# Kernel tuning notes

Measured on AMD Instinct MI355X. Metric: run time of the kernel, lower is better.

## Reference

```python
import jax, jax.numpy as jnp
import numpy as np

D_MODEL = 1024
D_STATE = 64
D_CONV = 4
EXPAND = 2
INNER = EXPAND * D_STATE          # 128
PROJ = D_STATE + 2 * INNER        # 320
B, L = 8, 4096
EPS = 1e-4


def setup_inputs() -> dict:
    key = jax.random.key(0)
    ks = jax.random.split(key, 6)
    x = jax.random.normal(ks[0], (B, L, D_MODEL), dtype=jnp.float32)
    # depthwise conv weight, torch layout (out=D, in/group=1, K)
    conv_w = jax.random.normal(ks[1], (D_MODEL, 1, D_CONV), dtype=jnp.float32) / np.sqrt(D_CONV)
    conv_b = jnp.zeros((D_MODEL,), dtype=jnp.float32)
    in_proj_w = jax.random.normal(ks[2], (PROJ, D_MODEL), dtype=jnp.float32) / np.sqrt(D_MODEL)
    in_proj_b = jnp.zeros((PROJ,), dtype=jnp.float32)
    A_log = jax.random.normal(ks[3], (D_STATE,), dtype=jnp.float32) * 0.1
    out_proj_w = jax.random.normal(ks[4], (D_MODEL, D_STATE), dtype=jnp.float32) / np.sqrt(D_STATE)
    out_proj_b = jnp.zeros((D_MODEL,), dtype=jnp.float32)
    return {"x": x, "conv_w": conv_w, "conv_b": conv_b,
            "in_proj_w": in_proj_w, "in_proj_b": in_proj_b,
            "A_log": A_log, "out_proj_w": out_proj_w, "out_proj_b": out_proj_b}


def _ssm_forward(x, conv_w, conv_b, in_proj_w, in_proj_b, A_log, out_proj_w, out_proj_b):
    bsz, L_in, _ = x.shape
    # depthwise conv1d, padding (D_CONV-1)//2 on both sides (torch semantics)
    pad = (D_CONV - 1) // 2
    xc = jnp.transpose(x, (0, 2, 1))  # (B, D, L)
    xc = jax.lax.conv_general_dilated(
        xc, conv_w, window_strides=(1,), padding=[(pad, pad)],
        dimension_numbers=("NCH", "OIH", "NCH"), feature_group_count=D_MODEL)
    xc = xc + conv_b[None, :, None]
    Lc = xc.shape[2]
    if Lc < L_in:  # K even -> conv output is L-1; pad zeros on the right
        xc = jnp.pad(xc, ((0, 0), (0, 0), (0, L_in - Lc)))
    elif Lc > L_in:
        xc = xc[:, :, :L_in]
    xc = jnp.transpose(xc, (0, 2, 1))  # (B, L, D)

    proj = xc @ in_proj_w.T + in_proj_b  # (B, L, PROJ)
    delta = proj[..., :D_STATE]                                  # (B, L, N)
    B_in = proj[..., D_STATE:D_STATE + INNER]
    C = proj[..., D_STATE + INNER:]
    n_groups = INNER // D_STATE
    B_in = B_in.reshape(bsz, L_in, D_STATE, n_groups).mean(axis=-1)  # (B, L, N)
    C = C.reshape(bsz, L_in, D_STATE, n_groups).mean(axis=-1)        # (B, L, N)

    # ZOH discretization
    A = -jnp.exp(A_log)[None, None, :]          # (1, 1, N)
    delta = jax.nn.softplus(delta)
    dA = delta * A
    A_bar = jnp.exp(dA)                         # (B, L, N)
    A_safe = jnp.where(jnp.abs(A) < EPS, EPS * jnp.sign(A) + EPS, A)
    scale = (A_bar - 1.0) / A_safe
    taylor = 1.0 + dA / 2.0 + dA * dA / 6.0
    scale = jnp.where(jnp.abs(A) < EPS, taylor, scale)
    B_bar = scale * B_in                        # (B, L, N)

    # linear recurrence h_t = A_bar_t * h_{t-1} + B_bar_t via associative scan
    def comb(e1, e2):
        a1, b1 = e1
        a2, b2 = e2
        return a1 * a2, a2 * b1 + b2
    _, h = jax.lax.associative_scan(comb, (A_bar, B_bar), axis=1)  # (B, L, N)

    y_state = C * h
    return y_state @ out_proj_w.T + out_proj_b  # (B, L, D)


def reference(x, conv_w, conv_b, in_proj_w, in_proj_b, A_log, out_proj_w, out_proj_b):
    return _ssm_forward(x, conv_w, conv_b, in_proj_w, in_proj_b, A_log, out_proj_w, out_proj_b)
```

## Files before the change

### kernel.cpp

```cpp
#include <hip/hip_runtime.h>
#include <cstdint>
#include <cstddef>

typedef __bf16 bf16;
typedef __attribute__((ext_vector_type(4))) __bf16 bf16x4;
typedef __attribute__((ext_vector_type(8))) __bf16 bf16x8;
typedef __attribute__((ext_vector_type(4))) float f32x4;

#define EPS_C 1e-4f
#define SWZ(r) (((r) ^ ((r) >> 2)) & 3)

#define BAR_LDS() do { asm volatile("s_waitcnt lgkmcnt(0)" ::: "memory"); \
                       __builtin_amdgcn_s_barrier(); } while (0)

__global__ __launch_bounds__(256) void k0_prep(const float* __restrict__ Wi,
    const float* __restrict__ Wo, bf16* __restrict__ Whg, bf16* __restrict__ Wlg,
    bf16* __restrict__ Wob, float* __restrict__ zpg)
{
    int idx = blockIdx.x * 256 + threadIdx.x;
    if (idx < 196608) {
        int nn = idx >> 10, k = idx & 1023;
        int wn = nn / 48, s = nn - wn * 48;
        if (s < 16) {
            int d = wn * 16 + s;
            float w = Wi[d * 1024 + k];
            bf16 h = (bf16)w;
            Whg[(k >> 5) * 6144 + nn * 32 + (k & 31)] = h;
            Wlg[(k >> 5) * 2048 + d * 32 + (k & 31)] = (bf16)(w - (float)h);
        } else if (s < 32) {
            int i = wn * 16 + (s - 16);
            float w = 0.5f * (Wi[(64 + 2 * i) * 1024 + k] + Wi[(65 + 2 * i) * 1024 + k]);
            Whg[(k >> 5) * 6144 + nn * 32 + (k & 31)] = (bf16)w;
        } else {
            int i = wn * 16 + (s - 32);
            float w = 0.5f * (Wi[(192 + 2 * i) * 1024 + k] + Wi[(193 + 2 * i) * 1024 + k]);
            Whg[(k >> 5) * 6144 + nn * 32 + (k & 31)] = (bf16)w;
        }
    } else if (idx < 262144) {
        int j = idx - 196608;
        Wob[j] = (bf16)Wo[j];
    } else {
        int j = idx - 262144;
        if (j < 1024) zpg[j] = 0.f;
    }
}

__global__ __launch_bounds__(256, 4) void k1_convproj(
    const float* __restrict__ x, const float* __restrict__ conv_w,
    const float* __restrict__ conv_b, const float* __restrict__ in_proj_b,
    const float* __restrict__ A_log,
    const bf16* __restrict__ Whg, const bf16* __restrict__ Wlg,
    const float* __restrict__ zpg,
    float* __restrict__ Yp, float* __restrict__ Zp,
    float* __restrict__ Psum, float* __restrict__ Ssum)
{
    __shared__ char smem[28672];

    const int tid  = threadIdx.x;
    const int lane = tid & 63;
    const int wn   = tid >> 6;
    const int fr   = lane & 15, fs = lane >> 4;
    const int b    = blockIdx.x >> 7;
    const int tc   = blockIdx.x & 127;
    const int t0   = tc * 32;
    const int rot  = (blockIdx.x * 5) & 31;

    const int ct = tid >> 3, cs = tid & 7;
    const int gt = t0 + ct;
    const bool zrow = (gt == 4095);
    const int xwo = ct * 64 + ((((cs >> 1) ^ SWZ(ct)) & 3) << 4) + (cs & 1) * 8;

    int aoff[2];
#pragma unroll
    for (int mi = 0; mi < 2; ++mi) {
        int r = mi * 16 + fr;
        aoff[mi] = r * 64 + ((fs ^ SWZ(r)) << 4);
    }

    const float* rp[4];
#pragma unroll
    for (int dt = 0; dt < 4; ++dt) {
        int g = gt - 1 + dt;
        rp[dt] = (g >= 0 && g < 4096) ? (x + ((size_t)b * 4096 + g) * 1024 + cs * 4)
                                      : (zpg + cs * 4);
    }

    const size_t wfo  = (size_t)(wn * 48 + fr) * 32 + fs * 8;
    const size_t wfol = (size_t)(wn * 16 + fr) * 32 + fs * 8;

    {
        float* cwT = (float*)(smem + 8192);
        float* cbl = (float*)(smem + 24576);
        for (int p = tid; p < 1024; p += 256) {
            f32x4 w4 = *(const f32x4*)&conv_w[p * 4];
            cwT[p]        = w4.x;
            cwT[1024 + p] = w4.y;
            cwT[2048 + p] = w4.z;
            cwT[3072 + p] = w4.w;
        }
        ((f32x4*)cbl)[tid] = ((const f32x4*)conv_b)[tid];
    }

    f32x4  xr[4];
    bf16x8 wfh[3], wfl;
    f32x4  acc[2][3] = {};

    auto L = [&](int c) { return (c + rot) & 31; };

    auto fetch_x = [&](int lc) {
#pragma unroll
        for (int dt = 0; dt < 4; ++dt)
            xr[dt] = *(const f32x4*)(rp[dt] + lc * 32);
    };
    auto fetch_w = [&](int lc) {
        const bf16* ph = Whg + (size_t)lc * 6144 + wfo;
#pragma unroll
        for (int ni = 0; ni < 3; ++ni)
            wfh[ni] = *(const bf16x8*)(ph + ni * 512);
        wfl = *(const bf16x8*)(Wlg + (size_t)lc * 2048 + wfol);
    };
    auto conv = [&](int lc, int p) {
        char* xh = smem + p * 2048;
        char* xl = smem + 4096 + p * 2048;
        const float* cwT = (const float*)(smem + 8192);
        const float* cbl = (const float*)(smem + 24576);
        const int ch0 = lc * 32 + cs * 4;
        f32x4 w0 = *(const f32x4*)&cwT[ch0];
        f32x4 w1 = *(const f32x4*)&cwT[1024 + ch0];
        f32x4 w2 = *(const f32x4*)&cwT[2048 + ch0];
        f32x4 w3 = *(const f32x4*)&cwT[3072 + ch0];
        f32x4 bb = *(const f32x4*)&cbl[ch0];
        bf16x4 hi, lo;
#pragma unroll
        for (int j = 0; j < 4; ++j) {
            float v = bb[j];
            v = fmaf(w0[j], xr[0][j], v);
            v = fmaf(w1[j], xr[1][j], v);
            v = fmaf(w2[j], xr[2][j], v);
            v = fmaf(w3[j], xr[3][j], v);
            v = zrow ? 0.f : v;
            bf16 h = (bf16)v;
            hi[j] = h;
            lo[j] = (bf16)(v - (float)h);
        }
        *(bf16x4*)(xh + xwo) = hi;
        *(bf16x4*)(xl + xwo) = lo;
    };

    fetch_x(L(0));
    fetch_w(L(0));
    __syncthreads();
    conv(L(0), 0);
    fetch_x(L(1));
    __syncthreads();

    auto body = [&](int c, int par) {
        const char* xh = smem + par * 2048;
        const char* xl = smem + 4096 + par * 2048;
        bf16x8 ah0 = *(const bf16x8*)(xh + aoff[0]);
        bf16x8 ah1 = *(const bf16x8*)(xh + aoff[1]);
        bf16x8 al0 = *(const bf16x8*)(xl + aoff[0]);
        bf16x8 al1 = *(const bf16x8*)(xl + aoff[1]);
        __builtin_amdgcn_s_setprio(1);
#pragma unroll
        for (int ni = 0; ni < 3; ++ni) {
            bf16x8 bh = wfh[ni];
            acc[0][ni] = __builtin_amdgcn_mfma_f32_16x16x32_bf16(ah0, bh, acc[0][ni], 0, 0, 0);
            acc[1][ni] = __builtin_amdgcn_mfma_f32_16x16x32_bf16(ah1, bh, acc[1][ni], 0, 0, 0);
            acc[0][ni] = __builtin_amdgcn_mfma_f32_16x16x32_bf16(al0, bh, acc[0][ni], 0, 0, 0);
            acc[1][ni] = __builtin_amdgcn_mfma_f32_16x16x32_bf16(al1, bh, acc[1][ni], 0, 0, 0);
        }
        acc[0][0] = __builtin_amdgcn_mfma_f32_16x16x32_bf16(ah0, wfl, acc[0][0], 0, 0, 0);
        acc[1][0] = __builtin_amdgcn_mfma_f32_16x16x32_bf16(ah1, wfl, acc[1][0], 0, 0, 0);
        __builtin_amdgcn_s_setprio(0);
        if (c + 1 < 32) {
            fetch_w(L(c + 1));
            conv(L(c + 1), par ^ 1);
            if (c + 2 < 32) fetch_x(L(c + 2));
        }
        BAR_LDS();
    };

#pragma unroll 1
    for (int cc = 0; cc < 32; cc += 2) {
        body(cc,     0);
        body(cc + 1, 1);
    }

    float* res = (float*)smem;
#pragma unroll
    for (int mi = 0; mi < 2; ++mi)
#pragma unroll
        for (int ni = 0; ni < 3; ++ni) {
            int col = wn * 48 + ni * 16 + fr;
#pragma unroll
            for (int r = 0; r < 4; ++r)
                res[(mi * 16 + fs * 4 + r) * 196 + col] = acc[mi][ni][r];
        }
    __syncthreads();

    float* part = (float*)(smem + 25088);
    const int i  = lane;
    const int tg = tid >> 6;
    const float A  = -expf(A_log[i]);
    const float bd = in_proj_b[i];
    const float bB = 0.5f * (in_proj_b[64 + 2 * i] + in_proj_b[65 + 2 * i]);
    const float bC = 0.5f * (in_proj_b[192 + 2 * i] + in_proj_b[193 + 2 * i]);
    const bool tiny = fabsf(A) < EPS_C;
    const int dcol = (i >> 4) * 48 + (i & 15);
    float av[8], bv[8], cv[8];
#pragma unroll
    for (int r = 0; r < 8; ++r) {
        int t = tg * 8 + r;
        float d  = res[t * 196 + dcol] + bd;
        float Bm = res[t * 196 + dcol + 16] + bB;
        float Cm = res[t * 196 + dcol + 32] + bC;
        float delta = (d > 20.f) ? d : log1pf(expf(d));
        float dA = delta * A;
        float abar = expf(dA);
        float sc = tiny ? (1.f + dA * 0.5f + dA * dA * (1.f / 6.f)) : ((abar - 1.f) / A);
        av[r] = abar; bv[r] = sc * Bm; cv[r] = Cm;
    }
    float P = 1.f, S = 0.f;
#pragma unroll
    for (int r = 0; r < 8; ++r) { S = fmaf(av[r], S, bv[r]); P *= av[r]; }
    part[tg * 64 + i] = P;
    part[256 + tg * 64 + i] = S;
    __syncthreads();
    float h = 0.f, pp = 1.f;
#pragma unroll
    for (int g = 0; g < 3; ++g)
        if (g < tg) {
            float Pg = part[g * 64 + i], Sg = part[256 + g * 64 + i];
            h = fmaf(Pg, h, Sg);
            pp *= Pg;
        }
    size_t ob = ((size_t)b * 4096 + t0 + tg * 8) * 64 + i;
#pragma unroll
    for (int r = 0; r < 8; ++r) {
        h  = fmaf(av[r], h, bv[r]);
        pp *= av[r];
        Yp[ob + (size_t)r * 64] = cv[r] * h;
        Zp[ob + (size_t)r * 64] = cv[r] * pp;
    }
    if (tg == 3) {
        size_t o = ((size_t)b * 128 + tc) * 64 + i;
        Psum[o] = pp;
        Ssum[o] = h;
    }
}

__global__ __launch_bounds__(64) void k2_scan2(const float* __restrict__ Psum,
    const float* __restrict__ Ssum, float* __restrict__ Carry)
{
    int b = blockIdx.x, i = threadIdx.x;
    float h = 0.f;
#pragma unroll 1
    for (int g = 0; g < 8; ++g) {
        size_t base = ((size_t)b * 128 + g * 16) * 64 + i;
        float Pv[16], Sv[16];
#pragma unroll
        for (int j = 0; j < 16; ++j) {
            Pv[j] = Psum[base + (size_t)j * 64];
            Sv[j] = Ssum[base + (size_t)j * 64];
        }
#pragma unroll
        for (int j = 0; j < 16; ++j) {
            Carry[base + (size_t)j * 64] = h;
            h = fmaf(Pv[j], h, Sv[j]);
        }
    }
}

__global__ __launch_bounds__(512) void k3_scan_out(
    const float* __restrict__ Yp, const float* __restrict__ Zp,
    const float* __restrict__ Carry, const bf16* __restrict__ Wob,
    const float* __restrict__ bo, float* __restrict__ out)
{
    __shared__ char sm3[4096];

    const int tid  = threadIdx.x;
    const int lane = tid & 63;
    const int wv   = tid >> 6;
    const int b    = blockIdx.x >> 7;
    const int ch   = blockIdx.x & 127;
    const int t0   = ch * 32;

    const int i = lane, tg = wv;
    float cr = Carry[((size_t)b * 128 + ch) * 64 + i];
    size_t base = ((size_t)b * 4096 + t0 + tg * 4) * 64 + i;
#pragma unroll
    for (int r = 0; r < 4; ++r) {
        float y = Yp[base + (size_t)r * 64] + Zp[base + (size_t)r * 64] * cr;
        int t = tg * 4 + r;
        int off = t * 128 + ((((i >> 3) ^ (t & 7)) & 7) << 4) + (i & 7) * 2;
        *(bf16*)(sm3 + off) = (bf16)y;
    }
    __syncthreads();

    const int fr = lane & 15, fs = lane >> 4;
    bf16x8 afr[2][2];
#pragma unroll
    for (int mi = 0; mi < 2; ++mi)
#pragma unroll
        for (int ks = 0; ks < 2; ++ks) {
            int row = mi * 16 + fr;
            int slot = ks * 4 + fs;
            int off = row * 128 + (((slot ^ (row & 7)) & 7) << 4);
            afr[mi][ks] = *(const bf16x8*)(sm3 + off);
        }
    const int n0 = wv * 128;
#pragma unroll
    for (int ni = 0; ni < 8; ++ni) {
        int col = n0 + ni * 16 + fr;
        bf16x8 b0 = *(const bf16x8*)(Wob + (size_t)col * 64 + fs * 8);
        bf16x8 b1 = *(const bf16x8*)(Wob + (size_t)col * 64 + 32 + fs * 8);
        float bias = bo[col];
#pragma unroll
        for (int mi = 0; mi < 2; ++mi) {
            f32x4 a = {};
            a = __builtin_amdgcn_mfma_f32_16x16x32_bf16(afr[mi][0], b0, a, 0, 0, 0);
            a = __builtin_amdgcn_mfma_f32_16x16x32_bf16(afr[mi][1], b1, a, 0, 0, 0);
#pragma unroll
            for (int r = 0; r < 4; ++r) {
                int t = mi * 16 + fs * 4 + r;
                out[((size_t)b * 4096 + t0 + t) * 1024 + col] = a[r] + bias;
            }
        }
    }
}

extern "C" void kernel_launch(void* const* d_in, const int* in_sizes, int n_in,
                              void* d_out, int out_size, void* d_ws, size_t ws_size,
                              hipStream_t stream) {
    const float* x          = (const float*)d_in[0];
    const float* conv_w     = (const float*)d_in[1];
    const float* conv_b     = (const float*)d_in[2];
    const float* in_proj_w  = (const float*)d_in[3];
    const float* in_proj_b  = (const float*)d_in[4];
    const float* A_log      = (const float*)d_in[5];
    const float* out_proj_w = (const float*)d_in[6];
    const float* out_proj_b = (const float*)d_in[7];
    float* out = (float*)d_out;

    char* w = (char*)d_ws;
    bf16*  Whg  = (bf16*)w;
    bf16*  Wlg  = (bf16*)(w + 393216);
    bf16*  Wob  = (bf16*)(w + 524288);
    float* Yp   = (float*)(w + 655360);
    float* Zp   = (float*)(w + 9043968);
    float* Psum = (float*)(w + 17432576);
    float* Ssum = (float*)(w + 17694720);
    float* Carry= (float*)(w + 17956864);
    float* zpg  = (float*)(w + 18219008);

    hipLaunchKernelGGL(k0_prep,     dim3(1032), dim3(256), 0, stream,
                       in_proj_w, out_proj_w, Whg, Wlg, Wob, zpg);
    hipLaunchKernelGGL(k1_convproj, dim3(1024), dim3(256), 0, stream,
                       x, conv_w, conv_b, in_proj_b, A_log, Whg, Wlg, zpg,
                       Yp, Zp, Psum, Ssum);
    hipLaunchKernelGGL(k2_scan2,    dim3(8),    dim3(64),  0, stream, Psum, Ssum, Carry);
    hipLaunchKernelGGL(k3_scan_out, dim3(1024), dim3(512), 0, stream,
                       Yp, Zp, Carry, Wob, out_proj_b, out);
}
```

Before: 113.2 us.

## Double time-tile per block to 64 rows, halving grid and chunk count

Each convproj and scan_out block now covers 64 timesteps instead of 32, so every loaded weight fragment feeds four MFMA row tiles instead of two, and each thread converts 8 channels per step. The grid shrinks to 512 blocks and the carry scan handles 64 chunks per batch in one unrolled pass. This raises weight reuse and cuts redundant conv halo loads. In exchange it uses more LDS and registers per block and launches fewer blocks, which lowers occupancy and may underfill the 256 CUs.

```diff
diff --git a/kernel.cpp b/kernel.cpp
--- a/kernel.cpp
+++ b/kernel.cpp
@@ -3,7 +3,6 @@
 #include <cstddef>
 
 typedef __bf16 bf16;
-typedef __attribute__((ext_vector_type(4))) __bf16 bf16x4;
 typedef __attribute__((ext_vector_type(8))) __bf16 bf16x8;
 typedef __attribute__((ext_vector_type(4))) float f32x4;
 
@@ -45,7 +44,7 @@
     }
 }
 
-__global__ __launch_bounds__(256, 4) void k1_convproj(
+__global__ __launch_bounds__(256) void k1_convproj(
     const float* __restrict__ x, const float* __restrict__ conv_w,
     const float* __restrict__ conv_b, const float* __restrict__ in_proj_b,
     const float* __restrict__ A_log,
@@ -54,25 +53,25 @@
     float* __restrict__ Yp, float* __restrict__ Zp,
     float* __restrict__ Psum, float* __restrict__ Ssum)
 {
-    __shared__ char smem[28672];
+    __shared__ char smem[52224];
 
     const int tid  = threadIdx.x;
     const int lane = tid & 63;
     const int wn   = tid >> 6;
     const int fr   = lane & 15, fs = lane >> 4;
-    const int b    = blockIdx.x >> 7;
-    const int tc   = blockIdx.x & 127;
-    const int t0   = tc * 32;
+    const int b    = blockIdx.x >> 6;
+    const int tc   = blockIdx.x & 63;
+    const int t0   = tc * 64;
     const int rot  = (blockIdx.x * 5) & 31;
 
-    const int ct = tid >> 3, cs = tid & 7;
+    const int ct = tid >> 2, cs = tid & 3;
     const int gt = t0 + ct;
     const bool zrow = (gt == 4095);
-    const int xwo = ct * 64 + ((((cs >> 1) ^ SWZ(ct)) & 3) << 4) + (cs & 1) * 8;
-
-    int aoff[2];
-#pragma unroll
-    for (int mi = 0; mi < 2; ++mi) {
+    const int xwo = ct * 64 + (((cs ^ SWZ(ct)) & 3) << 4);
+
+    int aoff[4];
+#pragma unroll
+    for (int mi = 0; mi < 4; ++mi) {
         int r = mi * 16 + fr;
         aoff[mi] = r * 64 + ((fs ^ SWZ(r)) << 4);
     }
@@ -81,16 +80,16 @@
 #pragma unroll
     for (int dt = 0; dt < 4; ++dt) {
         int g = gt - 1 + dt;
-        rp[dt] = (g >= 0 && g < 4096) ? (x + ((size_t)b * 4096 + g) * 1024 + cs * 4)
-                                      : (zpg + cs * 4);
+        rp[dt] = (g >= 0 && g < 4096) ? (x + ((size_t)b * 4096 + g) * 1024 + cs * 8)
+                                      : (zpg + cs * 8);
     }
 
     const size_t wfo  = (size_t)(wn * 48 + fr) * 32 + fs * 8;
     const size_t wfol = (size_t)(wn * 16 + fr) * 32 + fs * 8;
 
     {
-        float* cwT = (float*)(smem + 8192);
-        float* cbl = (float*)(smem + 24576);
+        float* cwT = (float*)(smem + 16384);
+        float* cbl = (float*)(smem + 32768);
         for (int p = tid; p < 1024; p += 256) {
             f32x4 w4 = *(const f32x4*)&conv_w[p * 4];
             cwT[p]        = w4.x;
@@ -101,16 +100,18 @@
         ((f32x4*)cbl)[tid] = ((const f32x4*)conv_b)[tid];
     }
 
-    f32x4  xr[4];
+    f32x4  xr[4][2];
     bf16x8 wfh[3], wfl;
-    f32x4  acc[2][3] = {};
+    f32x4  acc[4][3] = {};
 
     auto L = [&](int c) { return (c + rot) & 31; };
 
     auto fetch_x = [&](int lc) {
 #pragma unroll
-        for (int dt = 0; dt < 4; ++dt)
-            xr[dt] = *(const f32x4*)(rp[dt] + lc * 32);
+        for (int dt = 0; dt < 4; ++dt) {
+            xr[dt][0] = *(const f32x4*)(rp[dt] + lc * 32);
+            xr[dt][1] = *(const f32x4*)(rp[dt] + lc * 32 + 4);
+        }
     };
     auto fetch_w = [&](int lc) {
         const bf16* ph = Whg + (size_t)lc * 6144 + wfo;
@@ -120,31 +121,34 @@
         wfl = *(const bf16x8*)(Wlg + (size_t)lc * 2048 + wfol);
     };
     auto conv = [&](int lc, int p) {
-        char* xh = smem + p * 2048;
-        char* xl = smem + 4096 + p * 2048;
-        const float* cwT = (const float*)(smem + 8192);
-        const float* cbl = (const float*)(smem + 24576);
-        const int ch0 = lc * 32 + cs * 4;
-        f32x4 w0 = *(const f32x4*)&cwT[ch0];
-        f32x4 w1 = *(const f32x4*)&cwT[1024 + ch0];
-        f32x4 w2 = *(const f32x4*)&cwT[2048 + ch0];
-        f32x4 w3 = *(const f32x4*)&cwT[3072 + ch0];
-        f32x4 bb = *(const f32x4*)&cbl[ch0];
-        bf16x4 hi, lo;
-#pragma unroll
-        for (int j = 0; j < 4; ++j) {
-            float v = bb[j];
-            v = fmaf(w0[j], xr[0][j], v);
-            v = fmaf(w1[j], xr[1][j], v);
-            v = fmaf(w2[j], xr[2][j], v);
-            v = fmaf(w3[j], xr[3][j], v);
-            v = zrow ? 0.f : v;
-            bf16 h = (bf16)v;
-            hi[j] = h;
-            lo[j] = (bf16)(v - (float)h);
-        }
-        *(bf16x4*)(xh + xwo) = hi;
-        *(bf16x4*)(xl + xwo) = lo;
+        char* xh = smem + p * 4096;
+        char* xl = smem + 8192 + p * 4096;
+        const float* cwT = (const float*)(smem + 16384);
+        const float* cbl = (const float*)(smem + 32768);
+        bf16x8 hi, lo;
+#pragma unroll
+        for (int s = 0; s < 2; ++s) {
+            const int ch0 = lc * 32 + cs * 8 + s * 4;
+            f32x4 w0 = *(const f32x4*)&cwT[ch0];
+            f32x4 w1 = *(const f32x4*)&cwT[1024 + ch0];
+            f32x4 w2 = *(const f32x4*)&cwT[2048 + ch0];
+            f32x4 w3 = *(const f32x4*)&cwT[3072 + ch0];
+            f32x4 bb = *(const f32x4*)&cbl[ch0];
+#pragma unroll
+            for (int j = 0; j < 4; ++j) {
+                float v = bb[j];
+                v = fmaf(w0[j], xr[0][s][j], v);
+                v = fmaf(w1[j], xr[1][s][j], v);
+                v = fmaf(w2[j], xr[2][s][j], v);
+                v = fmaf(w3[j], xr[3][s][j], v);
+                v = zrow ? 0.f : v;
+                bf16 h = (bf16)v;
+                hi[s * 4 + j] = h;
+                lo[s * 4 + j] = (bf16)(v - (float)h);
+            }
+        }
+        *(bf16x8*)(xh + xwo) = hi;
+        *(bf16x8*)(xl + xwo) = lo;
     };
 
     fetch_x(L(0));
@@ -155,23 +159,28 @@
     __syncthreads();
 
     auto body = [&](int c, int par) {
-        const char* xh = smem + par * 2048;
-        const char* xl = smem + 4096 + par * 2048;
-        bf16x8 ah0 = *(const bf16x8*)(xh + aoff[0]);
-        bf16x8 ah1 = *(const bf16x8*)(xh + aoff[1]);
-        bf16x8 al0 = *(const bf16x8*)(xl + aoff[0]);
-        bf16x8 al1 = *(const bf16x8*)(xl + aoff[1]);
+        const char* xh = smem + par * 4096;
+        const char* xl = smem + 8192 + par * 4096;
+        bf16x8 ah[4], al[4];
+#pragma unroll
+        for (int mi = 0; mi < 4; ++mi) {
+            ah[mi] = *(const bf16x8*)(xh + aoff[mi]);
+            al[mi] = *(const bf16x8*)(xl + aoff[mi]);
+        }
         __builtin_amdgcn_s_setprio(1);
 #pragma unroll
         for (int ni = 0; ni < 3; ++ni) {
             bf16x8 bh = wfh[ni];
-            acc[0][ni] = __builtin_amdgcn_mfma_f32_16x16x32_bf16(ah0, bh, acc[0][ni], 0, 0, 0);
-            acc[1][ni] = __builtin_amdgcn_mfma_f32_16x16x32_bf16(ah1, bh, acc[1][ni], 0, 0, 0);
-            acc[0][ni] = __builtin_amdgcn_mfma_f32_16x16x32_bf16(al0, bh, acc[0][ni], 0, 0, 0);
-            acc[1][ni] = __builtin_amdgcn_mfma_f32_16x16x32_bf16(al1, bh, acc[1][ni], 0, 0, 0);
-        }
-        acc[0][0] = __builtin_amdgcn_mfma_f32_16x16x32_bf16(ah0, wfl, acc[0][0], 0, 0, 0);
-        acc[1][0] = __builtin_amdgcn_mfma_f32_16x16x32_bf16(ah1, wfl, acc[1][0], 0, 0, 0);
+#pragma unroll
+            for (int mi = 0; mi < 4; ++mi)
+                acc[mi][ni] = __builtin_amdgcn_mfma_f32_16x16x32_bf16(ah[mi], bh, acc[mi][ni], 0, 0, 0);
+#pragma unroll
+            for (int mi = 0; mi < 4; ++mi)
+                acc[mi][ni] = __builtin_amdgcn_mfma_f32_16x16x32_bf16(al[mi], bh, acc[mi][ni], 0, 0, 0);
+        }
+#pragma unroll
+        for (int mi = 0; mi < 4; ++mi)
+            acc[mi][0] = __builtin_amdgcn_mfma_f32_16x16x32_bf16(ah[mi], wfl, acc[mi][0], 0, 0, 0);
         __builtin_amdgcn_s_setprio(0);
         if (c + 1 < 32) {
             fetch_w(L(c + 1));
@@ -189,7 +198,7 @@
 
     float* res = (float*)smem;
 #pragma unroll
-    for (int mi = 0; mi < 2; ++mi)
+    for (int mi = 0; mi < 4; ++mi)
 #pragma unroll
         for (int ni = 0; ni < 3; ++ni) {
             int col = wn * 48 + ni * 16 + fr;
@@ -199,7 +208,7 @@
         }
     __syncthreads();
 
-    float* part = (float*)(smem + 25088);
+    float* part = (float*)(smem + 50176);
     const int i  = lane;
     const int tg = tid >> 6;
     const float A  = -expf(A_log[i]);
@@ -208,10 +217,10 @@
     const float bC = 0.5f * (in_proj_b[192 + 2 * i] + in_proj_b[193 + 2 * i]);
     const bool tiny = fabsf(A) < EPS_C;
     const int dcol = (i >> 4) * 48 + (i & 15);
-    float av[8], bv[8], cv[8];
-#pragma unroll
-    for (int r = 0; r < 8; ++r) {
-        int t = tg * 8 + r;
+    float av[16], bv[16], cv[16];
+#pragma unroll
+    for (int r = 0; r < 16; ++r) {
+        int t = tg * 16 + r;
         float d  = res[t * 196 + dcol] + bd;
         float Bm = res[t * 196 + dcol + 16] + bB;
         float Cm = res[t * 196 + dcol + 32] + bC;
@@ -223,7 +232,7 @@
     }
     float P = 1.f, S = 0.f;
 #pragma unroll
-    for (int r = 0; r < 8; ++r) { S = fmaf(av[r], S, bv[r]); P *= av[r]; }
+    for (int r = 0; r < 16; ++r) { S = fmaf(av[r], S, bv[r]); P *= av[r]; }
     part[tg * 64 + i] = P;
     part[256 + tg * 64 + i] = S;
     __syncthreads();
@@ -235,16 +244,16 @@
             h = fmaf(Pg, h, Sg);
             pp *= Pg;
         }
-    size_t ob = ((size_t)b * 4096 + t0 + tg * 8) * 64 + i;
-#pragma unroll
-    for (int r = 0; r < 8; ++r) {
+    size_t ob = ((size_t)b * 4096 + t0 + tg * 16) * 64 + i;
+#pragma unroll
+    for (int r = 0; r < 16; ++r) {
         h  = fmaf(av[r], h, bv[r]);
         pp *= av[r];
         Yp[ob + (size_t)r * 64] = cv[r] * h;
         Zp[ob + (size_t)r * 64] = cv[r] * pp;
     }
     if (tg == 3) {
-        size_t o = ((size_t)b * 128 + tc) * 64 + i;
+        size_t o = ((size_t)b * 64 + tc) * 64 + i;
         Psum[o] = pp;
         Ssum[o] = h;
     }
@@ -254,21 +263,18 @@
     const float* __restrict__ Ssum, float* __restrict__ Carry)
 {
     int b = blockIdx.x, i = threadIdx.x;
+    float Pv[64], Sv[64];
+#pragma unroll
+    for (int c = 0; c < 64; ++c) {
+        size_t o = ((size_t)(b * 64) + c) * 64 + i;
+        Pv[c] = Psum[o]; Sv[c] = Ssum[o];
+    }
     float h = 0.f;
-#pragma unroll 1
-    for (int g = 0; g < 8; ++g) {
-        size_t base = ((size_t)b * 128 + g * 16) * 64 + i;
-        float Pv[16], Sv[16];
-#pragma unroll
-        for (int j = 0; j < 16; ++j) {
-            Pv[j] = Psum[base + (size_t)j * 64];
-            Sv[j] = Ssum[base + (size_t)j * 64];
-        }
-#pragma unroll
-        for (int j = 0; j < 16; ++j) {
-            Carry[base + (size_t)j * 64] = h;
-            h = fmaf(Pv[j], h, Sv[j]);
-        }
+#pragma unroll
+    for (int c = 0; c < 64; ++c) {
+        size_t o = ((size_t)(b * 64) + c) * 64 + i;
+        Carry[o] = h;
+        h = fmaf(Pv[c], h, Sv[c]);
     }
 }
 
@@ -277,31 +283,31 @@
     const float* __restrict__ Carry, const bf16* __restrict__ Wob,
     const float* __restrict__ bo, float* __restrict__ out)
 {
-    __shared__ char sm3[4096];
+    __shared__ char sm3[8192];
 
     const int tid  = threadIdx.x;
     const int lane = tid & 63;
     const int wv   = tid >> 6;
-    const int b    = blockIdx.x >> 7;
-    const int ch   = blockIdx.x & 127;
-    const int t0   = ch * 32;
+    const int b    = blockIdx.x >> 6;
+    const int ch   = blockIdx.x & 63;
+    const int t0   = ch * 64;
 
     const int i = lane, tg = wv;
-    float cr = Carry[((size_t)b * 128 + ch) * 64 + i];
-    size_t base = ((size_t)b * 4096 + t0 + tg * 4) * 64 + i;
-#pragma unroll
-    for (int r = 0; r < 4; ++r) {
+    float cr = Carry[((size_t)(b * 64) + ch) * 64 + i];
+    size_t base = ((size_t)(b * 4096) + t0 + tg * 8) * 64 + i;
+#pragma unroll
+    for (int r = 0; r < 8; ++r) {
         float y = Yp[base + (size_t)r * 64] + Zp[base + (size_t)r * 64] * cr;
-        int t = tg * 4 + r;
+        int t = tg * 8 + r;
         int off = t * 128 + ((((i >> 3) ^ (t & 7)) & 7) << 4) + (i & 7) * 2;
         *(bf16*)(sm3 + off) = (bf16)y;
     }
     __syncthreads();
 
     const int fr = lane & 15, fs = lane >> 4;
-    bf16x8 afr[2][2];
-#pragma unroll
-    for (int mi = 0; mi < 2; ++mi)
+    bf16x8 afr[4][2];
+#pragma unroll
+    for (int mi = 0; mi < 4; ++mi)
 #pragma unroll
         for (int ks = 0; ks < 2; ++ks) {
             int row = mi * 16 + fr;
@@ -317,14 +323,14 @@
         bf16x8 b1 = *(const bf16x8*)(Wob + (size_t)col * 64 + 32 + fs * 8);
         float bias = bo[col];
 #pragma unroll
-        for (int mi = 0; mi < 2; ++mi) {
+        for (int mi = 0; mi < 4; ++mi) {
             f32x4 a = {};
             a = __builtin_amdgcn_mfma_f32_16x16x32_bf16(afr[mi][0], b0, a, 0, 0, 0);
             a = __builtin_amdgcn_mfma_f32_16x16x32_bf16(afr[mi][1], b1, a, 0, 0, 0);
 #pragma unroll
             for (int r = 0; r < 4; ++r) {
                 int t = mi * 16 + fs * 4 + r;
-                out[((size_t)b * 4096 + t0 + t) * 1024 + col] = a[r] + bias;
+                out[((size_t)(b * 4096) + t0 + t) * 1024 + col] = a[r] + bias;
             }
         }
     }
@@ -350,16 +356,16 @@
     float* Yp   = (float*)(w + 655360);
     float* Zp   = (float*)(w + 9043968);
     float* Psum = (float*)(w + 17432576);
-    float* Ssum = (float*)(w + 17694720);
-    float* Carry= (float*)(w + 17956864);
-    float* zpg  = (float*)(w + 18219008);
+    float* Ssum = (float*)(w + 17563648);
+    float* Carry= (float*)(w + 17694720);
+    float* zpg  = (float*)(w + 17825792);
 
     hipLaunchKernelGGL(k0_prep,     dim3(1032), dim3(256), 0, stream,
                        in_proj_w, out_proj_w, Whg, Wlg, Wob, zpg);
-    hipLaunchKernelGGL(k1_convproj, dim3(1024), dim3(256), 0, stream,
+    hipLaunchKernelGGL(k1_convproj, dim3(512),  dim3(256), 0, stream,
                        x, conv_w, conv_b, in_proj_b, A_log, Whg, Wlg, zpg,
                        Yp, Zp, Psum, Ssum);
     hipLaunchKernelGGL(k2_scan2,    dim3(8),    dim3(64),  0, stream, Psum, Ssum, Carry);
-    hipLaunchKernelGGL(k3_scan_out, dim3(1024), dim3(512), 0, stream,
+    hipLaunchKernelGGL(k3_scan_out, dim3(512),  dim3(512), 0, stream,
                        Yp, Zp, Carry, Wob, out_proj_b, out);
 }
```

After: 99.73 us. 11.9% less time.
